# Performance work log

Measured on AMD Instinct MI355X. Metric: run time of the kernel, lower is better.

Reference implementation:

```python
import jax, jax.numpy as jnp
import numpy as np

INPUT_DIM = 768
HIDDEN = 64
NUM_CLASSES = 1


def _uniform(key, shape, bound):
    return jax.random.uniform(key, shape, jnp.float32, -bound, bound)


def setup_inputs() -> dict:
    key = jax.random.key(0)
    ks = jax.random.split(key, 16)
    B, T = 128, 512
    bound = 1.0 / np.sqrt(HIDDEN)  # PyTorch RNN init range
    inp = {
        "x": jax.random.normal(ks[0], (B, T, INPUT_DIM), jnp.float32),
        "fixation_num": 1,
        # layer 0: input_dim -> hidden
        "W_ih0": _uniform(ks[1], (HIDDEN, INPUT_DIM), bound),
        "W_hh0": _uniform(ks[2], (HIDDEN, HIDDEN), bound),
        "b_ih0": _uniform(ks[3], (HIDDEN,), bound),
        "b_hh0": _uniform(ks[4], (HIDDEN,), bound),
        # layer 1
        "W_ih1": _uniform(ks[5], (HIDDEN, HIDDEN), bound),
        "W_hh1": _uniform(ks[6], (HIDDEN, HIDDEN), bound),
        "b_ih1": _uniform(ks[7], (HIDDEN,), bound),
        "b_hh1": _uniform(ks[8], (HIDDEN,), bound),
        # layer 2
        "W_ih2": _uniform(ks[9], (HIDDEN, HIDDEN), bound),
        "W_hh2": _uniform(ks[10], (HIDDEN, HIDDEN), bound),
        "b_ih2": _uniform(ks[11], (HIDDEN,), bound),
        "b_hh2": _uniform(ks[12], (HIDDEN,), bound),
        # final linear head
        "fc_w": _uniform(ks[13], (NUM_CLASSES, HIDDEN), bound),
        "fc_b": _uniform(ks[14], (NUM_CLASSES,), bound),
    }
    return inp


def _rnn_layer(x, W_ih, W_hh, b_ih, b_hh):
    # x: [B, T, In] -> hidden sequence [B, T, H]; vanilla tanh RNN, h0 = 0
    pre = jnp.einsum("bti,hi->bth", x, W_ih) + b_ih + b_hh  # input projection for all t
    B = x.shape[0]
    h0 = jnp.zeros((B, W_hh.shape[0]), x.dtype)

    def step(h, p_t):  # p_t: [B, H]
        h = jnp.tanh(p_t + h @ W_hh.T)
        return h, h

    _, hs = jax.lax.scan(step, h0, jnp.swapaxes(pre, 0, 1))  # hs: [T, B, H]
    return jnp.swapaxes(hs, 0, 1)


def reference(x, fixation_num, W_ih0, W_hh0, b_ih0, b_hh0,
              W_ih1, W_hh1, b_ih1, b_hh1,
              W_ih2, W_hh2, b_ih2, b_hh2, fc_w, fc_b):
    # fixation_num is unused by the original forward
    h = _rnn_layer(x, W_ih0, W_hh0, b_ih0, b_hh0)
    h = _rnn_layer(h, W_ih1, W_hh1, b_ih1, b_hh1)
    h = _rnn_layer(h, W_ih2, W_hh2, b_ih2, b_hh2)
    last = h[:, -1, :]  # [B, H]
    return last @ fc_w.T + fc_b  # [B, num_classes]
```

## Files before the change

kernel.cpp:

```cpp
#include <hip/hip_runtime.h>


typedef __fp16 h2_t __attribute__((ext_vector_type(2)));
typedef __fp16 h8_t __attribute__((ext_vector_type(8)));
typedef float  f4_t __attribute__((ext_vector_type(4)));

union F4H  { float4 f; h2_t h[4]; };
union F4H8 { float4 f; h8_t h8; h2_t h2[4]; };
union H8U  { h2_t h2[4]; h8_t h8; };

__device__ __forceinline__ float fdot2(h2_t a, h2_t b, float c) {
    return __builtin_amdgcn_fdot2(a, b, c, false);
}
__device__ __forceinline__ h2_t pack_h2(float x, float y) {
    return __builtin_amdgcn_cvt_pkrtz(x, y);
}
__device__ __forceinline__ float tanh_fast(float x) {
    float e = __expf(2.0f * x);
    return 1.0f - 2.0f * __builtin_amdgcn_rcpf(e + 1.0f);
}

__global__ __launch_bounds__(256) void pack_wih(
    const float* __restrict__ W, h8_t* __restrict__ wp)
{
    const int id = blockIdx.x * 256 + threadIdx.x;
    if (id >= 24 * 4 * 64) return;
    const int l  = id & 63;
    const int nt = (id >> 6) & 3;
    const int c  = id >> 8;
    const float* p = W + (size_t)(nt * 16 + (l & 15)) * 768 + c * 32 + (l >> 4) * 8;
    float4 r0 = *(const float4*)p;
    float4 r1 = *(const float4*)(p + 4);
    H8U u;
    u.h2[0] = pack_h2(r0.x, r0.y); u.h2[1] = pack_h2(r0.z, r0.w);
    u.h2[2] = pack_h2(r1.x, r1.y); u.h2[3] = pack_h2(r1.z, r1.w);
    wp[id] = u.h8;
}

__global__ __launch_bounds__(256) void gemm_pre0(
    const float* __restrict__ x,
    const h8_t* __restrict__ wp,
    const float* __restrict__ bih, const float* __restrict__ bhh,
    float* __restrict__ pre0)
{
    const int tid = threadIdx.x;
    const int wv  = tid >> 6;
    const int l   = tid & 63;
    const int m   = l & 15;
    const int q   = l >> 4;
    const int rowB = blockIdx.x * 64 + wv * 16;

    const float* ax = x + (size_t)(rowB + m) * 768 + q * 8;

    float4 ar[6][2];
    h8_t   bf[2][4];

#pragma unroll
    for (int c = 0; c < 6; ++c) {
        ar[c][0] = *(const float4*)(ax + c * 32);
        ar[c][1] = *(const float4*)(ax + c * 32 + 4);
    }
#pragma unroll
    for (int c = 0; c < 2; ++c) {
        const int cb = c * 256 + l;
        bf[c][0] = wp[cb];        bf[c][1] = wp[cb + 64];
        bf[c][2] = wp[cb + 128];  bf[c][3] = wp[cb + 192];
    }

    f4_t acc[4];
#pragma unroll
    for (int nt = 0; nt < 4; ++nt)
#pragma unroll
        for (int i = 0; i < 4; ++i) acc[nt][i] = 0.0f;

#pragma unroll
    for (int it = 0; it < 24; ++it) {
        const int as = it % 6;
        const int bs = it & 1;
        H8U fa;
        fa.h2[0] = pack_h2(ar[as][0].x, ar[as][0].y);
        fa.h2[1] = pack_h2(ar[as][0].z, ar[as][0].w);
        fa.h2[2] = pack_h2(ar[as][1].x, ar[as][1].y);
        fa.h2[3] = pack_h2(ar[as][1].z, ar[as][1].w);
        h8_t fb0 = bf[bs][0], fb1 = bf[bs][1], fb2 = bf[bs][2], fb3 = bf[bs][3];

        if (it + 6 < 24) {
            const int ko = (it + 6) * 32;
            ar[as][0] = *(const float4*)(ax + ko);
            ar[as][1] = *(const float4*)(ax + ko + 4);
        }
        if (it + 2 < 24) {
            const int cb = (it + 2) * 256 + l;
            bf[bs][0] = wp[cb];        bf[bs][1] = wp[cb + 64];
            bf[bs][2] = wp[cb + 128];  bf[bs][3] = wp[cb + 192];
        }

        acc[0] = __builtin_amdgcn_mfma_f32_16x16x32_f16(fa.h8, fb0, acc[0], 0, 0, 0);
        acc[1] = __builtin_amdgcn_mfma_f32_16x16x32_f16(fa.h8, fb1, acc[1], 0, 0, 0);
        acc[2] = __builtin_amdgcn_mfma_f32_16x16x32_f16(fa.h8, fb2, acc[2], 0, 0, 0);
        acc[3] = __builtin_amdgcn_mfma_f32_16x16x32_f16(fa.h8, fb3, acc[3], 0, 0, 0);
    }

    float bn[4];
#pragma unroll
    for (int nt = 0; nt < 4; ++nt) bn[nt] = bih[nt * 16 + m] + bhh[nt * 16 + m];
#pragma unroll
    for (int i = 0; i < 4; ++i) {
        int row = rowB + q * 4 + i;
        float* pr = pre0 + (size_t)row * 64 + m;
#pragma unroll
        for (int nt = 0; nt < 4; ++nt)
            pr[nt * 16] = acc[nt][i] + bn[nt];
    }
}

__device__ __forceinline__ float layer_epoch(
    const __fp16* __restrict__ in0,
    __fp16* __restrict__ self0, int par,
    const h2_t* wB2, const h8_t* wX, float* __restrict__ xb,
    const float* bias4, int j)
{
    __fp16*       selfPar  = self0 + par * 1024;
    const __fp16* selfPrev = self0 + (par ^ 1) * 1024;
    const int mm = j & 15;
    const int q4 = j >> 4;

    F4H8 A0, A1;
    const __fp16* arow = in0 + mm * 64 + q4 * 8;
    A0.f = *(const float4*)arow;
    A1.f = *(const float4*)(arow + 32);

    f4_t xacc[4];
#pragma unroll
    for (int nt = 0; nt < 4; ++nt) {
#pragma unroll
        for (int i = 0; i < 4; ++i) xacc[nt][i] = 0.0f;
        xacc[nt] = __builtin_amdgcn_mfma_f32_16x16x32_f16(
            A0.h8, wX[nt * 2 + 0], xacc[nt], 0, 0, 0);
        xacc[nt] = __builtin_amdgcn_mfma_f32_16x16x32_f16(
            A1.h8, wX[nt * 2 + 1], xacc[nt], 0, 0, 0);
    }
#pragma unroll
    for (int nt = 0; nt < 4; ++nt)
#pragma unroll
        for (int i = 0; i < 4; ++i)
            xb[(q4 * 4 + i) * 64 + nt * 16 + mm] = xacc[nt][i] + bias4[nt];

    float xs[16];
#pragma unroll
    for (int s = 0; s < 16; ++s) xs[s] = xb[s * 64 + j];

    float hN = 0.0f;
#pragma unroll
    for (int s = 0; s < 16; ++s) {
        const __fp16* rc = (s == 0) ? (selfPrev + 15 * 64) : (selfPar + (s - 1) * 64);
        F4H uh[8];
#pragma unroll
        for (int qq = 0; qq < 8; ++qq) uh[qq].f = *(const float4*)(rc + qq * 8);

        float a0 = 0.f, a1 = 0.f, a2 = 0.f, a3 = 0.f;
#pragma unroll
        for (int qq = 0; qq < 8; ++qq) {
            a0 = fdot2(wB2[qq * 4 + 0], uh[qq].h[0], a0);
            a1 = fdot2(wB2[qq * 4 + 1], uh[qq].h[1], a1);
            a2 = fdot2(wB2[qq * 4 + 2], uh[qq].h[2], a2);
            a3 = fdot2(wB2[qq * 4 + 3], uh[qq].h[3], a3);
        }
        hN = tanh_fast((a0 + a1) + (a2 + a3) + xs[s]);
        selfPar[s * 64 + j] = (__fp16)hN;
    }
    return hN;
}

__global__ __launch_bounds__(192, 1) void rnn_fused(
    const float* __restrict__ pre0,
    const float* __restrict__ Whh0,
    const float* __restrict__ Wih1, const float* __restrict__ Whh1,
    const float* __restrict__ bih1, const float* __restrict__ bhh1,
    const float* __restrict__ Wih2, const float* __restrict__ Whh2,
    const float* __restrict__ bih2, const float* __restrict__ bhh2,
    const float* __restrict__ fcw, const float* __restrict__ fcb,
    float* __restrict__ out)
{
    const int tid = threadIdx.x;
    const int g   = tid >> 6;
    const int j   = tid & 63;
    const int b   = blockIdx.x;

    __shared__ __align__(16) __fp16 hb[3][2][16][64];
    __shared__ __align__(16) float  xb2[2][16][64];

    const float* WB = (g == 0) ? Whh0 : ((g == 1) ? Whh1 : Whh2);
    h2_t wB2[32];
#pragma unroll
    for (int i = 0; i < 32; ++i)
        wB2[i] = pack_h2(WB[j * 64 + 2 * i], WB[j * 64 + 2 * i + 1]);

    const float* WX = (g == 1) ? Wih1 : ((g == 2) ? Wih2 : Whh0);
    const int mm = j & 15, q4 = j >> 4;
    h8_t wX[8];
#pragma unroll
    for (int nt = 0; nt < 4; ++nt)
#pragma unroll
        for (int c = 0; c < 2; ++c) {
            const float* p = WX + (nt * 16 + mm) * 64 + c * 32 + q4 * 8;
            float4 r0 = *(const float4*)p;
            float4 r1 = *(const float4*)(p + 4);
            H8U u;
            u.h2[0] = pack_h2(r0.x, r0.y); u.h2[1] = pack_h2(r0.z, r0.w);
            u.h2[2] = pack_h2(r1.x, r1.y); u.h2[3] = pack_h2(r1.z, r1.w);
            wX[nt * 2 + c] = u.h8;
        }

    float bias4[4];
#pragma unroll
    for (int nt = 0; nt < 4; ++nt) {
        const int col = nt * 16 + mm;
        bias4[nt] = (g == 1) ? (bih1[col] + bhh1[col])
                  : ((g == 2) ? (bih2[col] + bhh2[col]) : 0.0f);
    }

#pragma unroll
    for (int i = 0; i < 16; ++i) ((unsigned int*)hb)[tid + 192 * i] = 0u;

    const size_t pbase = (size_t)b * 32768;
    float pc[16], pn[16];
    if (g == 0) {
#pragma unroll
        for (int s = 0; s < 16; ++s) pc[s] = pre0[pbase + s * 64 + j];
    }
    __syncthreads();

    float hLast = 0.0f;

    for (int e = 0; e < 34; ++e) {
        if (g == 0) {
            if (e < 32) {
                if (e < 31) {
#pragma unroll
                    for (int s = 0; s < 16; ++s)
                        pn[s] = pre0[pbase + (size_t)(e + 1) * 1024 + s * 64 + j];
                }
                const int par = e & 1;
#pragma unroll
                for (int s = 0; s < 16; ++s) {
                    const __fp16* rc = (s == 0) ? hb[0][par ^ 1][15] : hb[0][par][s - 1];
                    float a0 = 0.f, a1 = 0.f, a2 = 0.f, a3 = 0.f;
#pragma unroll
                    for (int qq = 0; qq < 8; ++qq) {
                        F4H u; u.f = *(const float4*)&rc[qq * 8];
                        a0 = fdot2(wB2[qq * 4 + 0], u.h[0], a0);
                        a1 = fdot2(wB2[qq * 4 + 1], u.h[1], a1);
                        a2 = fdot2(wB2[qq * 4 + 2], u.h[2], a2);
                        a3 = fdot2(wB2[qq * 4 + 3], u.h[3], a3);
                    }
                    float hN = tanh_fast((a0 + a1) + (a2 + a3) + pc[s]);
                    hb[0][par][s][j] = (__fp16)hN;
                }
#pragma unroll
                for (int s = 0; s < 16; ++s) pc[s] = pn[s];
            }
        } else if (g == 1) {
            if (e >= 1 && e < 33) {
                const int par = (e - 1) & 1;
                layer_epoch(&hb[0][par][0][0], &hb[1][0][0][0], par,
                            wB2, wX, &xb2[0][0][0], bias4, j);
            }
        } else {
            if (e >= 2) {
                const int par = e & 1;
                float hN = layer_epoch(&hb[1][par][0][0], &hb[2][0][0][0], par,
                                       wB2, wX, &xb2[1][0][0], bias4, j);
                if (e == 33) hLast = hN;
            }
        }
        __syncthreads();
    }

    if (g == 2) {
        float v = hLast * fcw[j];
#pragma unroll
        for (int m = 1; m < 64; m <<= 1) v += __shfl_xor(v, m, 64);
        if (j == 0) out[b] = v + fcb[0];
    }
}

extern "C" void kernel_launch(void* const* d_in, const int* in_sizes, int n_in,
                              void* d_out, int out_size, void* d_ws, size_t ws_size,
                              hipStream_t stream) {
    const float* x    = (const float*)d_in[0];
    const float* Wih0 = (const float*)d_in[2];
    const float* Whh0 = (const float*)d_in[3];
    const float* bih0 = (const float*)d_in[4];
    const float* bhh0 = (const float*)d_in[5];
    const float* Wih1 = (const float*)d_in[6];
    const float* Whh1 = (const float*)d_in[7];
    const float* bih1 = (const float*)d_in[8];
    const float* bhh1 = (const float*)d_in[9];
    const float* Wih2 = (const float*)d_in[10];
    const float* Whh2 = (const float*)d_in[11];
    const float* bih2 = (const float*)d_in[12];
    const float* bhh2 = (const float*)d_in[13];
    const float* fcw  = (const float*)d_in[14];
    const float* fcb  = (const float*)d_in[15];
    float* out  = (float*)d_out;
    float* pre0 = (float*)d_ws;
    h8_t* wpack = (h8_t*)((char*)d_ws + (size_t)65536 * 64 * 4);

    pack_wih<<<24, 256, 0, stream>>>(Wih0, wpack);
    gemm_pre0<<<1024, 256, 0, stream>>>(x, wpack, bih0, bhh0, pre0);
    rnn_fused<<<128, 192, 0, stream>>>(pre0, Whh0, Wih1, Whh1, bih1, bhh1,
                                       Wih2, Whh2, bih2, bhh2, fcw, fcb, out);
}
```

Before: 411.0 us.

## Fuse input-projection GEMM into recurrent kernel with per-chunk flag synchronization

Merges the layer-0 input projection GEMM and the three-layer recurrent kernel into one launch. The first 128 blocks run the recurrence and the remaining 1024 blocks compute pre-activation tiles, each publishing a release flag. Recurrent blocks spin on the flag for each 4-epoch chunk, so the serial recurrence can start before the whole GEMM finishes. It relies on the GEMM blocks being scheduled concurrently with the recurrent blocks to avoid deadlock or stalls. Recurrent blocks also grow from 192 to 256 threads with one idle wave.

Result: slower. 511.0 us (+24.3%).

```diff
diff --git a/kernel.cpp b/kernel.cpp
--- a/kernel.cpp
+++ b/kernel.cpp
@@ -20,10 +20,18 @@
     return 1.0f - 2.0f * __builtin_amdgcn_rcpf(e + 1.0f);
 }
 
+__device__ __forceinline__ void wait_flag(const int* f) {
+    if (__hip_atomic_load(f, __ATOMIC_ACQUIRE, __HIP_MEMORY_SCOPE_AGENT)) return;
+    while (__hip_atomic_load(f, __ATOMIC_RELAXED, __HIP_MEMORY_SCOPE_AGENT) == 0)
+        __builtin_amdgcn_s_sleep(4);
+    (void)__hip_atomic_load(f, __ATOMIC_ACQUIRE, __HIP_MEMORY_SCOPE_AGENT);
+}
+
 __global__ __launch_bounds__(256) void pack_wih(
-    const float* __restrict__ W, h8_t* __restrict__ wp)
+    const float* __restrict__ W, h8_t* __restrict__ wp, int* __restrict__ flags)
 {
     const int id = blockIdx.x * 256 + threadIdx.x;
+    if (id < 1024) flags[id] = 0;
     if (id >= 24 * 4 * 64) return;
     const int l  = id & 63;
     const int nt = (id >> 6) & 3;
@@ -37,83 +45,6 @@
     wp[id] = u.h8;
 }
 
-__global__ __launch_bounds__(256) void gemm_pre0(
-    const float* __restrict__ x,
-    const h8_t* __restrict__ wp,
-    const float* __restrict__ bih, const float* __restrict__ bhh,
-    float* __restrict__ pre0)
-{
-    const int tid = threadIdx.x;
-    const int wv  = tid >> 6;
-    const int l   = tid & 63;
-    const int m   = l & 15;
-    const int q   = l >> 4;
-    const int rowB = blockIdx.x * 64 + wv * 16;
-
-    const float* ax = x + (size_t)(rowB + m) * 768 + q * 8;
-
-    float4 ar[6][2];
-    h8_t   bf[2][4];
-
-#pragma unroll
-    for (int c = 0; c < 6; ++c) {
-        ar[c][0] = *(const float4*)(ax + c * 32);
-        ar[c][1] = *(const float4*)(ax + c * 32 + 4);
-    }
-#pragma unroll
-    for (int c = 0; c < 2; ++c) {
-        const int cb = c * 256 + l;
-        bf[c][0] = wp[cb];        bf[c][1] = wp[cb + 64];
-        bf[c][2] = wp[cb + 128];  bf[c][3] = wp[cb + 192];
-    }
-
-    f4_t acc[4];
-#pragma unroll
-    for (int nt = 0; nt < 4; ++nt)
-#pragma unroll
-        for (int i = 0; i < 4; ++i) acc[nt][i] = 0.0f;
-
-#pragma unroll
-    for (int it = 0; it < 24; ++it) {
-        const int as = it % 6;
-        const int bs = it & 1;
-        H8U fa;
-        fa.h2[0] = pack_h2(ar[as][0].x, ar[as][0].y);
-        fa.h2[1] = pack_h2(ar[as][0].z, ar[as][0].w);
-        fa.h2[2] = pack_h2(ar[as][1].x, ar[as][1].y);
-        fa.h2[3] = pack_h2(ar[as][1].z, ar[as][1].w);
-        h8_t fb0 = bf[bs][0], fb1 = bf[bs][1], fb2 = bf[bs][2], fb3 = bf[bs][3];
-
-        if (it + 6 < 24) {
-            const int ko = (it + 6) * 32;
-            ar[as][0] = *(const float4*)(ax + ko);
-            ar[as][1] = *(const float4*)(ax + ko + 4);
-        }
-        if (it + 2 < 24) {
-            const int cb = (it + 2) * 256 + l;
-            bf[bs][0] = wp[cb];        bf[bs][1] = wp[cb + 64];
-            bf[bs][2] = wp[cb + 128];  bf[bs][3] = wp[cb + 192];
-        }
-
-        acc[0] = __builtin_amdgcn_mfma_f32_16x16x32_f16(fa.h8, fb0, acc[0], 0, 0, 0);
-        acc[1] = __builtin_amdgcn_mfma_f32_16x16x32_f16(fa.h8, fb1, acc[1], 0, 0, 0);
-        acc[2] = __builtin_amdgcn_mfma_f32_16x16x32_f16(fa.h8, fb2, acc[2], 0, 0, 0);
-        acc[3] = __builtin_amdgcn_mfma_f32_16x16x32_f16(fa.h8, fb3, acc[3], 0, 0, 0);
-    }
-
-    float bn[4];
-#pragma unroll
-    for (int nt = 0; nt < 4; ++nt) bn[nt] = bih[nt * 16 + m] + bhh[nt * 16 + m];
-#pragma unroll
-    for (int i = 0; i < 4; ++i) {
-        int row = rowB + q * 4 + i;
-        float* pr = pre0 + (size_t)row * 64 + m;
-#pragma unroll
-        for (int nt = 0; nt < 4; ++nt)
-            pr[nt * 16] = acc[nt][i] + bn[nt];
-    }
-}
-
 __device__ __forceinline__ float layer_epoch(
     const __fp16* __restrict__ in0,
     __fp16* __restrict__ self0, int par,
@@ -172,8 +103,12 @@
     return hN;
 }
 
-__global__ __launch_bounds__(192, 1) void rnn_fused(
-    const float* __restrict__ pre0,
+__global__ __launch_bounds__(256) void fused_rnn(
+    const float* __restrict__ x,
+    const h8_t* __restrict__ wp,
+    const float* __restrict__ bih0, const float* __restrict__ bhh0,
+    float* __restrict__ pre0,
+    int* __restrict__ flags,
     const float* __restrict__ Whh0,
     const float* __restrict__ Wih1, const float* __restrict__ Whh1,
     const float* __restrict__ bih1, const float* __restrict__ bhh1,
@@ -182,50 +117,136 @@
     const float* __restrict__ fcw, const float* __restrict__ fcb,
     float* __restrict__ out)
 {
+    __shared__ __align__(16) __fp16 hb[3][2][16][64];
+    __shared__ __align__(16) float  xb2[2][16][64];
+
     const int tid = threadIdx.x;
+
+    if (blockIdx.x >= 128) {
+        const int gb  = blockIdx.x - 128;
+        const int wv  = tid >> 6;
+        const int l   = tid & 63;
+        const int m   = l & 15;
+        const int q   = l >> 4;
+        const int rowB = gb * 64 + wv * 16;
+
+        const float* ax = x + (size_t)(rowB + m) * 768 + q * 8;
+
+        float4 ar[6][2];
+        h8_t   bf[2][4];
+
+#pragma unroll
+        for (int c = 0; c < 6; ++c) {
+            ar[c][0] = *(const float4*)(ax + c * 32);
+            ar[c][1] = *(const float4*)(ax + c * 32 + 4);
+        }
+#pragma unroll
+        for (int c = 0; c < 2; ++c) {
+            const int cb = c * 256 + l;
+            bf[c][0] = wp[cb];        bf[c][1] = wp[cb + 64];
+            bf[c][2] = wp[cb + 128];  bf[c][3] = wp[cb + 192];
+        }
+
+        f4_t acc[4];
+#pragma unroll
+        for (int nt = 0; nt < 4; ++nt)
+#pragma unroll
+            for (int i = 0; i < 4; ++i) acc[nt][i] = 0.0f;
+
+#pragma unroll
+        for (int it = 0; it < 24; ++it) {
+            const int as = it % 6;
+            const int bs = it & 1;
+            H8U fa;
+            fa.h2[0] = pack_h2(ar[as][0].x, ar[as][0].y);
+            fa.h2[1] = pack_h2(ar[as][0].z, ar[as][0].w);
+            fa.h2[2] = pack_h2(ar[as][1].x, ar[as][1].y);
+            fa.h2[3] = pack_h2(ar[as][1].z, ar[as][1].w);
+            h8_t fb0 = bf[bs][0], fb1 = bf[bs][1], fb2 = bf[bs][2], fb3 = bf[bs][3];
+
+            if (it + 6 < 24) {
+                const int ko = (it + 6) * 32;
+                ar[as][0] = *(const float4*)(ax + ko);
+                ar[as][1] = *(const float4*)(ax + ko + 4);
+            }
+            if (it + 2 < 24) {
+                const int cb = (it + 2) * 256 + l;
+                bf[bs][0] = wp[cb];        bf[bs][1] = wp[cb + 64];
+                bf[bs][2] = wp[cb + 128];  bf[bs][3] = wp[cb + 192];
+            }
+
+            acc[0] = __builtin_amdgcn_mfma_f32_16x16x32_f16(fa.h8, fb0, acc[0], 0, 0, 0);
+            acc[1] = __builtin_amdgcn_mfma_f32_16x16x32_f16(fa.h8, fb1, acc[1], 0, 0, 0);
+            acc[2] = __builtin_amdgcn_mfma_f32_16x16x32_f16(fa.h8, fb2, acc[2], 0, 0, 0);
+            acc[3] = __builtin_amdgcn_mfma_f32_16x16x32_f16(fa.h8, fb3, acc[3], 0, 0, 0);
+        }
+
+        float bn[4];
+#pragma unroll
+        for (int nt = 0; nt < 4; ++nt) bn[nt] = bih0[nt * 16 + m] + bhh0[nt * 16 + m];
+#pragma unroll
+        for (int i = 0; i < 4; ++i) {
+            int row = rowB + q * 4 + i;
+            float* pr = pre0 + (size_t)row * 64 + m;
+#pragma unroll
+            for (int nt = 0; nt < 4; ++nt)
+                pr[nt * 16] = acc[nt][i] + bn[nt];
+        }
+
+        __syncthreads();
+        if (tid == 0) {
+            __threadfence();
+            __hip_atomic_store(&flags[gb], 1, __ATOMIC_RELEASE,
+                               __HIP_MEMORY_SCOPE_AGENT);
+        }
+        return;
+    }
+
     const int g   = tid >> 6;
     const int j   = tid & 63;
     const int b   = blockIdx.x;
-
-    __shared__ __align__(16) __fp16 hb[3][2][16][64];
-    __shared__ __align__(16) float  xb2[2][16][64];
-
-    const float* WB = (g == 0) ? Whh0 : ((g == 1) ? Whh1 : Whh2);
+    const int* myflags = flags + 8 * b;
+
     h2_t wB2[32];
-#pragma unroll
-    for (int i = 0; i < 32; ++i)
-        wB2[i] = pack_h2(WB[j * 64 + 2 * i], WB[j * 64 + 2 * i + 1]);
-
-    const float* WX = (g == 1) ? Wih1 : ((g == 2) ? Wih2 : Whh0);
+    h8_t wX[8];
+    float bias4[4];
     const int mm = j & 15, q4 = j >> 4;
-    h8_t wX[8];
-#pragma unroll
-    for (int nt = 0; nt < 4; ++nt)
-#pragma unroll
-        for (int c = 0; c < 2; ++c) {
-            const float* p = WX + (nt * 16 + mm) * 64 + c * 32 + q4 * 8;
-            float4 r0 = *(const float4*)p;
-            float4 r1 = *(const float4*)(p + 4);
-            H8U u;
-            u.h2[0] = pack_h2(r0.x, r0.y); u.h2[1] = pack_h2(r0.z, r0.w);
-            u.h2[2] = pack_h2(r1.x, r1.y); u.h2[3] = pack_h2(r1.z, r1.w);
-            wX[nt * 2 + c] = u.h8;
-        }
-
-    float bias4[4];
-#pragma unroll
-    for (int nt = 0; nt < 4; ++nt) {
-        const int col = nt * 16 + mm;
-        bias4[nt] = (g == 1) ? (bih1[col] + bhh1[col])
-                  : ((g == 2) ? (bih2[col] + bhh2[col]) : 0.0f);
-    }
-
-#pragma unroll
-    for (int i = 0; i < 16; ++i) ((unsigned int*)hb)[tid + 192 * i] = 0u;
+
+    if (g < 3) {
+        const float* WB = (g == 0) ? Whh0 : ((g == 1) ? Whh1 : Whh2);
+#pragma unroll
+        for (int i = 0; i < 32; ++i)
+            wB2[i] = pack_h2(WB[j * 64 + 2 * i], WB[j * 64 + 2 * i + 1]);
+
+        const float* WX = (g == 1) ? Wih1 : ((g == 2) ? Wih2 : Whh0);
+#pragma unroll
+        for (int nt = 0; nt < 4; ++nt)
+#pragma unroll
+            for (int c = 0; c < 2; ++c) {
+                const float* p = WX + (nt * 16 + mm) * 64 + c * 32 + q4 * 8;
+                float4 r0 = *(const float4*)p;
+                float4 r1 = *(const float4*)(p + 4);
+                H8U u;
+                u.h2[0] = pack_h2(r0.x, r0.y); u.h2[1] = pack_h2(r0.z, r0.w);
+                u.h2[2] = pack_h2(r1.x, r1.y); u.h2[3] = pack_h2(r1.z, r1.w);
+                wX[nt * 2 + c] = u.h8;
+            }
+
+#pragma unroll
+        for (int nt = 0; nt < 4; ++nt) {
+            const int col = nt * 16 + mm;
+            bias4[nt] = (g == 1) ? (bih1[col] + bhh1[col])
+                      : ((g == 2) ? (bih2[col] + bhh2[col]) : 0.0f);
+        }
+    }
+
+#pragma unroll
+    for (int i = 0; i < 12; ++i) ((unsigned int*)hb)[tid + 256 * i] = 0u;
 
     const size_t pbase = (size_t)b * 32768;
     float pc[16], pn[16];
     if (g == 0) {
+        wait_flag(myflags + 0);
 #pragma unroll
         for (int s = 0; s < 16; ++s) pc[s] = pre0[pbase + s * 64 + j];
     }
@@ -237,6 +258,7 @@
         if (g == 0) {
             if (e < 32) {
                 if (e < 31) {
+                    if (((e + 1) & 3) == 0) wait_flag(myflags + ((e + 1) >> 2));
 #pragma unroll
                     for (int s = 0; s < 16; ++s)
                         pn[s] = pre0[pbase + (size_t)(e + 1) * 1024 + s * 64 + j];
@@ -266,7 +288,7 @@
                 layer_epoch(&hb[0][par][0][0], &hb[1][0][0][0], par,
                             wB2, wX, &xb2[0][0][0], bias4, j);
             }
-        } else {
+        } else if (g == 2) {
             if (e >= 2) {
                 const int par = e & 1;
                 float hN = layer_epoch(&hb[1][par][0][0], &hb[2][0][0][0], par,
@@ -280,7 +302,7 @@
     if (g == 2) {
         float v = hLast * fcw[j];
 #pragma unroll
-        for (int m = 1; m < 64; m <<= 1) v += __shfl_xor(v, m, 64);
+        for (int m2 = 1; m2 < 64; m2 <<= 1) v += __shfl_xor(v, m2, 64);
         if (j == 0) out[b] = v + fcb[0];
     }
 }
@@ -306,9 +328,10 @@
     float* out  = (float*)d_out;
     float* pre0 = (float*)d_ws;
     h8_t* wpack = (h8_t*)((char*)d_ws + (size_t)65536 * 64 * 4);
-
-    pack_wih<<<24, 256, 0, stream>>>(Wih0, wpack);
-    gemm_pre0<<<1024, 256, 0, stream>>>(x, wpack, bih0, bhh0, pre0);
-    rnn_fused<<<128, 192, 0, stream>>>(pre0, Whh0, Wih1, Whh1, bih1, bhh1,
-                                       Wih2, Whh2, bih2, bhh2, fcw, fcb, out);
-}
+    int*  flags = (int*)((char*)d_ws + (size_t)65536 * 64 * 4 + 98304);
+
+    pack_wih<<<24, 256, 0, stream>>>(Wih0, wpack, flags);
+    fused_rnn<<<1152, 256, 0, stream>>>(x, wpack, bih0, bhh0, pre0, flags,
+                                        Whh0, Wih1, Whh1, bih1, bhh1,
+                                        Wih2, Whh2, bih2, bhh2, fcw, fcb, out);
+}
```
